# Kernel optimization log

Hardware: AMD Instinct MI355X
Metric: run time of the kernel (lower is better)

The kernel has to match this reference:

```python
import jax, jax.numpy as jnp
import numpy as np

IN_DIM = 64
OUT_DIM = 64
NUM_HEADS = 4
NEG_SLOPE = 0.2
GAMMA = 1.0  # constraint_gamma
NUM_VARS = 100000
NUM_CLAUSES = 100000
NUM_CLUSTERS = 2048
VARS_PER = 64
CLAUSES_PER = 64
NUM_EDGES = 400000


def _xavier(k, shape):
    bound = np.sqrt(6.0 / (shape[0] + shape[1])).astype(np.float32)
    return jax.random.uniform(k, shape, jnp.float32, -bound, bound)


def setup_inputs() -> dict:
    key = jax.random.key(0)
    ks = jax.random.split(key, 11)
    return {
        "x_var": jax.random.normal(ks[0], (NUM_VARS, IN_DIM), jnp.float32),
        "x_clause": jax.random.normal(ks[1], (NUM_CLAUSES, IN_DIM), jnp.float32),
        "var_clause_edge_index": jax.random.randint(ks[2], (2, NUM_EDGES), 0, NUM_VARS),
        "edge_polarity": jax.random.normal(ks[3], (NUM_EDGES, 1), jnp.float32),
        "cluster_var_ids": jax.random.randint(ks[4], (NUM_CLUSTERS, VARS_PER), 0, NUM_VARS),
        "cluster_clause_ids": jax.random.randint(ks[5], (NUM_CLUSTERS, CLAUSES_PER), 0, NUM_CLAUSES),
        "satisfaction_scores": jax.random.uniform(ks[6], (NUM_CLAUSES,), jnp.float32),
        "active_heads": 4,
        "W_Q": _xavier(ks[7], (OUT_DIM, IN_DIM)),
        "W_K": _xavier(ks[8], (OUT_DIM, IN_DIM)),
        "W_V": _xavier(ks[9], (OUT_DIM, IN_DIM)),
        "head_weights": jnp.ones((NUM_HEADS,), jnp.float32),
        "out_proj_w": _xavier(ks[10], (OUT_DIM, OUT_DIM)),
        "out_proj_b": jnp.zeros((OUT_DIM,), jnp.float32),
    }


def reference(x_var, x_clause, var_clause_edge_index, edge_polarity,
              cluster_var_ids, cluster_clause_ids, satisfaction_scores,
              active_heads, W_Q, W_K, W_V, head_weights, out_proj_w, out_proj_b):
    # NOTE: var_clause_edge_index / edge_polarity are accepted but unused,
    # matching the original forward body.
    num_vars = x_var.shape[0]
    x_all = jnp.concatenate([x_var, x_clause], axis=0)            # [N, D]
    Q = x_all @ W_Q.T
    K = x_all @ W_K.T
    V = x_all @ W_V.T

    # Block-diagonal cluster layout: [C, S] with S = VARS_PER + CLAUSES_PER
    nodes = jnp.concatenate([cluster_var_ids, cluster_clause_ids + num_vars], axis=1)
    Qc = Q[nodes]                                                 # [C, S, D]
    Kc = K[nodes]
    Vc = V[nodes]

    scale = jnp.asarray(np.sqrt(OUT_DIM), Qc.dtype)
    scores = jnp.einsum('csd,ctd->cst', Qc, Kc) / scale            # [C, S, S]
    # constraint-aware bias on clause columns (added before leaky_relu)
    bias = jnp.concatenate(
        [jnp.zeros(cluster_var_ids.shape, scores.dtype),
         GAMMA * satisfaction_scores[cluster_clause_ids]], axis=1)  # [C, S]
    scores = jax.nn.leaky_relu(scores + bias[:, None, :], NEG_SLOPE)
    attn = jax.nn.softmax(scores, axis=-1)

    head_w = jnp.mean(head_weights[:active_heads])
    h = jnp.einsum('cst,ctd->csd', attn, Vc) * head_w             # [C, S, D]

    flat = nodes.reshape(-1)
    out = jnp.zeros_like(x_all).at[flat].add(h.reshape(-1, OUT_DIM))
    count = jnp.zeros((x_all.shape[0],), x_all.dtype).at[flat].add(1.0)
    out = out / jnp.maximum(count, 1.0)[:, None]
    out = out @ out_proj_w.T + out_proj_b

    return (x_var + out[:num_vars], x_clause + out[num_vars:])
```

## Files before the change

kernel.cpp:

```cpp
#include <hip/hip_runtime.h>


#define NV 100000
#define NN 200000
#define NCLUST 2048
#define XS 72
#define AS 136

typedef __attribute__((ext_vector_type(8))) short short8;
typedef __attribute__((ext_vector_type(16))) float floatx16;

__device__ __forceinline__ unsigned short f2bf(float f) {
    union { float f; unsigned u; } v; v.f = f;
    unsigned r = v.u + 0x7fffu + ((v.u >> 16) & 1u);
    return (unsigned short)(r >> 16);
}
__device__ __forceinline__ int crow(int r, int lane) {
    return (r & 3) + 8 * (r >> 2) + 4 * (lane >> 5);
}

__global__ __launch_bounds__(256) void prep_kernel(
    const float* __restrict__ WQ, const float* __restrict__ WK,
    const float* __restrict__ WV, const float* __restrict__ Wout,
    const float* __restrict__ head_weights, const int* __restrict__ active_heads_p,
    unsigned short* __restrict__ Mtr, unsigned short* __restrict__ Pbf)
{
    int o = blockIdx.x * blockDim.x + threadIdx.x;
    int ah = active_heads_p[0];
    float hw = 0.f;
    for (int i = 0; i < ah; ++i) hw += head_weights[i];
    hw /= (float)ah;
    if (o < 4096) {
        int d = o >> 6, a = o & 63;
        float acc = 0.f;
        for (int j = 0; j < 64; ++j) acc += WQ[j*64 + a] * WK[j*64 + d];
        Mtr[o] = f2bf(acc * 0.125f);
    } else if (o < 8192) {
        int o2 = o - 4096;
        int j = o2 >> 6, b = o2 & 63;
        float acc = 0.f;
        for (int d = 0; d < 64; ++d) acc += Wout[j*64 + d] * WV[d*64 + b];
        Pbf[o2] = f2bf(acc * hw);
    }
}

__global__ __launch_bounds__(256, 3) void attn_kernel(
    const float* __restrict__ x_var, const float* __restrict__ x_clause,
    const int* __restrict__ cvar, const int* __restrict__ ccl,
    const float* __restrict__ sat, const unsigned short* __restrict__ Mtr,
    float* __restrict__ accum, float* __restrict__ countv)
{
    __shared__ union {
        struct { unsigned short Zc[128 * XS]; unsigned short Xc[128 * XS]; } s;
        unsigned short attn[128 * AS];
    } u;
    __shared__ unsigned short XcT[64 * AS];

    const int tid = threadIdx.x, lane = tid & 63, w = tid >> 6;
    const int c = blockIdx.x;
    const int m = lane & 31, hk = (lane >> 5) * 8;

    short8 mb0[4], mb1[4];
    #pragma unroll
    for (int ks = 0; ks < 4; ++ks) {
        mb0[ks] = *(const short8*)(Mtr + m * 64 + ks * 16 + hk);
        mb1[ks] = *(const short8*)(Mtr + (32 + m) * 64 + ks * 16 + hk);
    }

    {
        const int r = tid >> 1, half = tid & 1;
        int nid;
        const float* src;
        if (r < 64) {
            nid = cvar[c * 64 + r];
            src = x_var + (size_t)nid * 64;
        } else {
            int cid = ccl[c * 64 + (r - 64)];
            nid = NV + cid;
            src = x_clause + (size_t)cid * 64;
            if (half) *(float*)&XcT[(r - 64) * AS + 132] = sat[cid];
        }
        if (!half) ((int*)&XcT[(r >> 1) * AS + 128])[r & 1] = nid;
        union { unsigned short us[32]; short8 v[4]; } hb;
        const float4* s4 = (const float4*)src + half * 8;
        #pragma unroll
        for (int i = 0; i < 8; ++i) {
            float4 v = s4[i];
            hb.us[i*4+0] = f2bf(v.x); hb.us[i*4+1] = f2bf(v.y);
            hb.us[i*4+2] = f2bf(v.z); hb.us[i*4+3] = f2bf(v.w);
        }
        const int c0 = half * 32;
        #pragma unroll
        for (int i = 0; i < 4; ++i) *(short8*)&u.s.Xc[r * XS + c0 + i * 8] = hb.v[i];
        #pragma unroll
        for (int i = 0; i < 32; ++i) XcT[(c0 + i) * AS + r] = hb.us[i];
    }
    __syncthreads();
    if (tid < 128)
        atomicAdd(&countv[((const int*)&XcT[(tid >> 1) * AS + 128])[tid & 1]], 1.0f);

    floatx16 z0 = {}, z1 = {};
    #pragma unroll
    for (int ks = 0; ks < 4; ++ks) {
        short8 a = *(const short8*)&u.s.Xc[(w * 32 + m) * XS + ks * 16 + hk];
        z0 = __builtin_amdgcn_mfma_f32_32x32x16_bf16(a, mb0[ks], z0, 0, 0, 0);
        z1 = __builtin_amdgcn_mfma_f32_32x32x16_bf16(a, mb1[ks], z1, 0, 0, 0);
    }
    #pragma unroll
    for (int r = 0; r < 16; ++r) {
        int row = w * 32 + crow(r, lane);
        u.s.Zc[row * XS + m]      = f2bf(z0[r]);
        u.s.Zc[row * XS + 32 + m] = f2bf(z1[r]);
    }

    floatx16 sc[4] = {{}, {}, {}, {}};
    #pragma unroll
    for (int ks = 0; ks < 4; ++ks) {
        short8 a = *(const short8*)&u.s.Zc[(w * 32 + m) * XS + ks * 16 + hk];
        #pragma unroll
        for (int nt = 0; nt < 4; ++nt) {
            short8 b = *(const short8*)&u.s.Xc[(nt * 32 + m) * XS + ks * 16 + hk];
            sc[nt] = __builtin_amdgcn_mfma_f32_32x32x16_bf16(a, b, sc[nt], 0, 0, 0);
        }
    }

    const float b2 = *(const float*)&XcT[m * AS + 132];
    const float b3 = *(const float*)&XcT[(32 + m) * AS + 132];
    #pragma unroll
    for (int r = 0; r < 16; ++r) {
        float a0 = sc[0][r], a1 = sc[1][r], a2 = sc[2][r] + b2, a3 = sc[3][r] + b3;
        a0 = a0 > 0.f ? a0 : 0.2f * a0;
        a1 = a1 > 0.f ? a1 : 0.2f * a1;
        a2 = a2 > 0.f ? a2 : 0.2f * a2;
        a3 = a3 > 0.f ? a3 : 0.2f * a3;
        sc[0][r] = __expf(a0); sc[1][r] = __expf(a1);
        sc[2][r] = __expf(a2); sc[3][r] = __expf(a3);
    }

    __syncthreads();

    #pragma unroll
    for (int r = 0; r < 16; ++r) {
        int row = w * 32 + crow(r, lane);
        u.attn[row * AS + m]      = f2bf(sc[0][r]);
        u.attn[row * AS + 32 + m] = f2bf(sc[1][r]);
        u.attn[row * AS + 64 + m] = f2bf(sc[2][r]);
        u.attn[row * AS + 96 + m] = f2bf(sc[3][r]);
    }

    const short8 vones = (short8)(short)0x3F80;
    floatx16 g0 = {}, g1 = {}, rs = {};
    #pragma unroll
    for (int ks = 0; ks < 8; ++ks) {
        short8 a  = *(const short8*)&u.attn[(w * 32 + m) * AS + ks * 16 + hk];
        short8 b0 = *(const short8*)&XcT[m * AS + ks * 16 + hk];
        short8 b1 = *(const short8*)&XcT[(32 + m) * AS + ks * 16 + hk];
        g0 = __builtin_amdgcn_mfma_f32_32x32x16_bf16(a, b0, g0, 0, 0, 0);
        g1 = __builtin_amdgcn_mfma_f32_32x32x16_bf16(a, b1, g1, 0, 0, 0);
        rs = __builtin_amdgcn_mfma_f32_32x32x16_bf16(a, vones, rs, 0, 0, 0);
    }

    #pragma unroll
    for (int r = 0; r < 16; ++r) {
        int row = w * 32 + crow(r, lane);
        int nid = ((const int*)&XcT[(row >> 1) * AS + 128])[row & 1];
        float inv = __builtin_amdgcn_rcpf(rs[r]);
        float* base = accum + (size_t)nid * 64;
        atomicAdd(base + m,      g0[r] * inv);
        atomicAdd(base + 32 + m, g1[r] * inv);
    }
}

__global__ __launch_bounds__(256, 4) void finalize_kernel(
    const float* __restrict__ x_var, const float* __restrict__ x_clause,
    const float* __restrict__ accum, const float* __restrict__ countv,
    const unsigned short* __restrict__ Pbf, const float* __restrict__ bout,
    float* __restrict__ out)
{
    __shared__ unsigned short G[256 * XS];
    const int tid = threadIdx.x, lane = tid & 63, w = tid >> 6;
    const int base = blockIdx.x * 256;

    #pragma unroll 4
    for (int it = 0; it < 32; ++it) {
        int idx2 = it * 256 + tid;
        int lrow = idx2 >> 5, col2 = idx2 & 31;
        int n = base + lrow;
        float2 v = make_float2(0.f, 0.f);
        float cnt = 1.f;
        if (n < NN) {
            v = *(const float2*)(accum + (size_t)n * 64 + col2 * 2);
            cnt = countv[n];
        }
        float inv = 1.0f / fmaxf(cnt, 1.0f);
        unsigned pk = (unsigned)f2bf(v.x * inv) | ((unsigned)f2bf(v.y * inv) << 16);
        *(unsigned*)&G[lrow * XS + col2 * 2] = pk;
    }
    __syncthreads();

    const int m = lane & 31, hk = (lane >> 5) * 8;
    short8 pb[2][4];
    #pragma unroll
    for (int nt = 0; nt < 2; ++nt)
        #pragma unroll
        for (int ks = 0; ks < 4; ++ks)
            pb[nt][ks] = *(const short8*)(Pbf + (nt * 32 + m) * 64 + ks * 16 + hk);
    const float bias0 = bout[m], bias1 = bout[32 + m];

    #pragma unroll
    for (int tm = 0; tm < 2; ++tm) {
        int mt = w * 2 + tm;
        floatx16 c0 = {}, c1 = {};
        #pragma unroll
        for (int ks = 0; ks < 4; ++ks) {
            short8 a = *(const short8*)&G[(mt * 32 + m) * XS + ks * 16 + hk];
            c0 = __builtin_amdgcn_mfma_f32_32x32x16_bf16(a, pb[0][ks], c0, 0, 0, 0);
            c1 = __builtin_amdgcn_mfma_f32_32x32x16_bf16(a, pb[1][ks], c1, 0, 0, 0);
        }
        #pragma unroll
        for (int r = 0; r < 16; ++r) {
            int n = base + mt * 32 + crow(r, lane);
            if (n < NN) {
                const float* xs = (n < NV) ? (x_var + (size_t)n * 64)
                                           : (x_clause + (size_t)(n - NV) * 64);
                out[(size_t)n * 64 + m]      = xs[m]      + c0[r] + bias0;
                out[(size_t)n * 64 + 32 + m] = xs[32 + m] + c1[r] + bias1;
            }
        }
    }
}

extern "C" void kernel_launch(void* const* d_in, const int* in_sizes, int n_in,
                              void* d_out, int out_size, void* d_ws, size_t ws_size,
                              hipStream_t stream)
{
    const float* x_var        = (const float*)d_in[0];
    const float* x_clause     = (const float*)d_in[1];
    const int*   cvar         = (const int*)d_in[4];
    const int*   ccl          = (const int*)d_in[5];
    const float* sat          = (const float*)d_in[6];
    const int*   active_heads = (const int*)d_in[7];
    const float* WQ           = (const float*)d_in[8];
    const float* WK           = (const float*)d_in[9];
    const float* WV           = (const float*)d_in[10];
    const float* head_weights = (const float*)d_in[11];
    const float* Wout         = (const float*)d_in[12];
    const float* bout         = (const float*)d_in[13];

    float* accum  = (float*)d_ws;
    float* countv = accum + (size_t)NN * 64;
    unsigned short* Mtr = (unsigned short*)(countv + NN);
    unsigned short* Pbf = Mtr + 4096;

    hipMemsetAsync(accum, 0, (size_t)(NN * 64 + NN) * sizeof(float), stream);
    prep_kernel<<<32, 256, 0, stream>>>(WQ, WK, WV, Wout, head_weights, active_heads, Mtr, Pbf);
    attn_kernel<<<NCLUST, 256, 0, stream>>>(x_var, x_clause, cvar, ccl, sat, Mtr, accum, countv);
    finalize_kernel<<<(NN + 255) / 256, 256, 0, stream>>>(x_var, x_clause, accum, countv, Pbf, bout, (float*)d_out);
}
```

Before: 252.9 us.

## Accumulate scatter results in bf16 with packed atomics and read directly in finalize

```diff
diff --git a/kernel.cpp b/kernel.cpp
--- a/kernel.cpp
+++ b/kernel.cpp
@@ -48,7 +48,7 @@
     const float* __restrict__ x_var, const float* __restrict__ x_clause,
     const int* __restrict__ cvar, const int* __restrict__ ccl,
     const float* __restrict__ sat, const unsigned short* __restrict__ Mtr,
-    float* __restrict__ accum, float* __restrict__ countv)
+    unsigned short* __restrict__ accum_bf, float* __restrict__ countv)
 {
     __shared__ union {
         struct { unsigned short Zc[128 * XS]; unsigned short Xc[128 * XS]; } s;
@@ -160,41 +160,38 @@
         rs = __builtin_amdgcn_mfma_f32_32x32x16_bf16(a, vones, rs, 0, 0, 0);
     }
 
+    const bool ev = !(lane & 1);
+    const int colbase = ev ? m : (31 + m);
     #pragma unroll
     for (int r = 0; r < 16; ++r) {
         int row = w * 32 + crow(r, lane);
         int nid = ((const int*)&XcT[(row >> 1) * AS + 128])[row & 1];
         float inv = __builtin_amdgcn_rcpf(rs[r]);
-        float* base = accum + (size_t)nid * 64;
-        atomicAdd(base + m,      g0[r] * inv);
-        atomicAdd(base + 32 + m, g1[r] * inv);
+        float a0 = g0[r] * inv, a1 = g1[r] * inv;
+        float t0 = __shfl_xor(a0, 1, 64);
+        float t1 = __shfl_xor(a1, 1, 64);
+        float lo = ev ? a0 : t1;
+        float hi = ev ? t0 : a1;
+        unsigned pk = (unsigned)f2bf(lo) | ((unsigned)f2bf(hi) << 16);
+        unsigned long long addr =
+            (unsigned long long)(accum_bf + (size_t)nid * 64 + colbase);
+        asm volatile("global_atomic_pk_add_bf16 %0, %1, off"
+                     :: "v"(addr), "v"(pk) : "memory");
     }
 }
 
 __global__ __launch_bounds__(256, 4) void finalize_kernel(
     const float* __restrict__ x_var, const float* __restrict__ x_clause,
-    const float* __restrict__ accum, const float* __restrict__ countv,
+    const unsigned short* __restrict__ accum_bf, const float* __restrict__ countv,
     const unsigned short* __restrict__ Pbf, const float* __restrict__ bout,
     float* __restrict__ out)
 {
-    __shared__ unsigned short G[256 * XS];
+    __shared__ float cnts[256];
     const int tid = threadIdx.x, lane = tid & 63, w = tid >> 6;
     const int base = blockIdx.x * 256;
-
-    #pragma unroll 4
-    for (int it = 0; it < 32; ++it) {
-        int idx2 = it * 256 + tid;
-        int lrow = idx2 >> 5, col2 = idx2 & 31;
-        int n = base + lrow;
-        float2 v = make_float2(0.f, 0.f);
-        float cnt = 1.f;
-        if (n < NN) {
-            v = *(const float2*)(accum + (size_t)n * 64 + col2 * 2);
-            cnt = countv[n];
-        }
-        float inv = 1.0f / fmaxf(cnt, 1.0f);
-        unsigned pk = (unsigned)f2bf(v.x * inv) | ((unsigned)f2bf(v.y * inv) << 16);
-        *(unsigned*)&G[lrow * XS + col2 * 2] = pk;
+    {
+        int n = base + tid;
+        cnts[tid] = (n < NN) ? countv[n] : 1.f;
     }
     __syncthreads();
 
@@ -210,21 +207,24 @@
     #pragma unroll
     for (int tm = 0; tm < 2; ++tm) {
         int mt = w * 2 + tm;
+        const unsigned short* arow = accum_bf + (size_t)(base + mt * 32 + m) * 64;
         floatx16 c0 = {}, c1 = {};
         #pragma unroll
         for (int ks = 0; ks < 4; ++ks) {
-            short8 a = *(const short8*)&G[(mt * 32 + m) * XS + ks * 16 + hk];
+            short8 a = *(const short8*)(arow + ks * 16 + hk);
             c0 = __builtin_amdgcn_mfma_f32_32x32x16_bf16(a, pb[0][ks], c0, 0, 0, 0);
             c1 = __builtin_amdgcn_mfma_f32_32x32x16_bf16(a, pb[1][ks], c1, 0, 0, 0);
         }
         #pragma unroll
         for (int r = 0; r < 16; ++r) {
-            int n = base + mt * 32 + crow(r, lane);
+            int lrow = mt * 32 + crow(r, lane);
+            int n = base + lrow;
             if (n < NN) {
+                float inv = 1.0f / fmaxf(cnts[lrow], 1.0f);
                 const float* xs = (n < NV) ? (x_var + (size_t)n * 64)
                                            : (x_clause + (size_t)(n - NV) * 64);
-                out[(size_t)n * 64 + m]      = xs[m]      + c0[r] + bias0;
-                out[(size_t)n * 64 + 32 + m] = xs[32 + m] + c1[r] + bias1;
+                out[(size_t)n * 64 + m]      = xs[m]      + c0[r] * inv + bias0;
+                out[(size_t)n * 64 + 32 + m] = xs[32 + m] + c1[r] * inv + bias1;
             }
         }
     }
@@ -247,13 +247,13 @@
     const float* Wout         = (const float*)d_in[12];
     const float* bout         = (const float*)d_in[13];
 
-    float* accum  = (float*)d_ws;
-    float* countv = accum + (size_t)NN * 64;
+    unsigned short* accum_bf = (unsigned short*)d_ws;
+    float* countv = (float*)(accum_bf + (size_t)NN * 64);
     unsigned short* Mtr = (unsigned short*)(countv + NN);
     unsigned short* Pbf = Mtr + 4096;
 
-    hipMemsetAsync(accum, 0, (size_t)(NN * 64 + NN) * sizeof(float), stream);
+    hipMemsetAsync(accum_bf, 0, (size_t)NN * 64 * 2 + (size_t)NN * 4, stream);
     prep_kernel<<<32, 256, 0, stream>>>(WQ, WK, WV, Wout, head_weights, active_heads, Mtr, Pbf);
-    attn_kernel<<<NCLUST, 256, 0, stream>>>(x_var, x_clause, cvar, ccl, sat, Mtr, accum, countv);
-    finalize_kernel<<<(NN + 255) / 256, 256, 0, stream>>>(x_var, x_clause, accum, countv, Pbf, bout, (float*)d_out);
-}
+    attn_kernel<<<NCLUST, 256, 0, stream>>>(x_var, x_clause, cvar, ccl, sat, Mtr, accum_bf, countv);
+    finalize_kernel<<<(NN + 255) / 256, 256, 0, stream>>>(x_var, x_clause, accum_bf, countv, Pbf, bout, (float*)d_out);
+}
```

Result: faster. 214.6 us (-15.1%).
